# Optimization experiments

Measured on AMD Instinct MI355X. Metric: run time of the kernel, lower is better.

Reference implementation:

```python
import jax, jax.numpy as jnp
import numpy as np

B, N, F_IN, F_OUT, E = 8, 4096, 256, 256, 131072


def setup_inputs() -> dict:
    key = jax.random.key(0)
    kx, ke, kw = jax.random.split(key, 3)
    x = jax.random.normal(kx, (B, N, F_IN), dtype=jnp.float32)
    edge_index = jax.random.randint(ke, (2, E), 0, N, dtype=jnp.int32)
    # Xavier-uniform init for weight, zeros for bias (matches reset_parameters)
    limit = float(np.sqrt(6.0 / (F_IN + F_OUT)))
    weight = jax.random.uniform(kw, (F_IN, F_OUT), dtype=jnp.float32,
                                minval=-limit, maxval=limit)
    bias = jnp.zeros((F_OUT,), dtype=jnp.float32)
    return {"x": x, "edge_index": edge_index, "weight": weight, "bias": bias}


def reference(x, edge_index, weight, bias):
    # x: (B, N, F_in) -> transformed: (B, N, F_out)
    xt = jnp.einsum("bnf,fo->bno", x, weight)
    n_nodes = x.shape[1]
    # Adjacency is identical for every batch element in the original
    # (built from the same edge_index inside the loop) -> build once.
    # .set(1.0) matches torch's `adj[src, dst] = 1.0` (duplicates collapse).
    adj = jnp.zeros((n_nodes, n_nodes), dtype=xt.dtype)
    adj = adj.at[edge_index[0], edge_index[1]].set(1.0)
    degree = adj.sum(axis=1, keepdims=True) + 1e-6  # (N, 1)
    adj_norm = adj / degree
    # Aggregate: out[b] = adj_norm @ xt[b], batched as one einsum
    out = jnp.einsum("ij,bjf->bif", adj_norm, xt)
    return out + bias
```

## Files before the change

### kernel.cpp

```cpp
#include <hip/hip_runtime.h>
#include <hip/hip_bf16.h>


#define GC_B     8
#define GC_N     4096
#define GC_F     256
#define GC_E     131072
#define GC_M     (GC_B * GC_N)
#define MASK_WPR (GC_N / 32)
#define LIST_CAP 128

typedef __attribute__((ext_vector_type(8))) short         short8;
typedef __attribute__((ext_vector_type(2))) float         float2v;
typedef __attribute__((ext_vector_type(4))) float         float4v;
typedef __attribute__((ext_vector_type(4))) unsigned int  uint4v;

static __device__ __forceinline__ unsigned short f2bf_rne(float f) {
    unsigned u = __builtin_bit_cast(unsigned, f);
    u += 0x7fffu + ((u >> 16) & 1u);
    return (unsigned short)(u >> 16);
}

static __device__ __forceinline__ float2v bfpair(unsigned v) {
    return (float2v){__builtin_bit_cast(float, v << 16),
                     __builtin_bit_cast(float, v)};
}

__global__ __launch_bounds__(256) void prep_kernel(
        const float* __restrict__ X, const float* __restrict__ W,
        unsigned short* __restrict__ Xb, unsigned short* __restrict__ Wt,
        unsigned* __restrict__ mask, unsigned* __restrict__ cnt) {
    const int blk = blockIdx.x;
    const int t   = threadIdx.x;
    if (blk < 4096) {
        const size_t i = ((size_t)blk * 256 + t) * 8;
        const float4v v0 = *(const float4v*)(X + i);
        const float4v v1 = *(const float4v*)(X + i + 4);
        union { unsigned short h[8]; short8 s; } u;
        u.h[0] = f2bf_rne(v0[0]); u.h[1] = f2bf_rne(v0[1]);
        u.h[2] = f2bf_rne(v0[2]); u.h[3] = f2bf_rne(v0[3]);
        u.h[4] = f2bf_rne(v1[0]); u.h[5] = f2bf_rne(v1[1]);
        u.h[6] = f2bf_rne(v1[2]); u.h[7] = f2bf_rne(v1[3]);
        *(short8*)(Xb + i) = u.s;
    } else if (blk < 4352) {
        const int n = blk - 4096;
        Wt[n * GC_F + t] = f2bf_rne(W[t * GC_F + n]);
    } else if (blk < 4480) {
        const size_t base = ((size_t)(blk - 4352) * 256 + t) * 4;
        const uint4v z = {0, 0, 0, 0};
        #pragma unroll
        for (int j = 0; j < 4; j++) ((uint4v*)mask)[base + j] = z;
    } else {
        const uint4v z = {0, 0, 0, 0};
        #pragma unroll
        for (int j = 0; j < 4; j++) ((uint4v*)cnt)[(size_t)t * 4 + j] = z;
    }
}

__global__ void build_list_kernel(const int* __restrict__ ei,
                                  unsigned* __restrict__ mask,
                                  unsigned* __restrict__ cnt,
                                  unsigned short* __restrict__ list) {
    const int e = blockIdx.x * blockDim.x + threadIdx.x;
    if (e < GC_E) {
        const int s = ei[e];
        const int d = ei[GC_E + e];
        const unsigned bit = 1u << (d & 31);
        const unsigned old = atomicOr(&mask[s * MASK_WPR + (d >> 5)], bit);
        if (!(old & bit)) {
            const unsigned p = atomicAdd(&cnt[s], 1u);
            if (p < LIST_CAP) list[s * LIST_CAP + p] = (unsigned short)d;
        }
    }
}

__global__ __launch_bounds__(256) void aggregate_kernel(
        const unsigned short* __restrict__ Xb, const unsigned* __restrict__ cnt,
        const unsigned short* __restrict__ list,
        unsigned short* __restrict__ aggb) {
    __shared__ unsigned short lst[4][LIST_CAP];
    __shared__ int degs[4];

    const int w    = threadIdx.x >> 6;
    const int lane = threadIdx.x & 63;
    const int b    = blockIdx.x & 7;
    const int i    = (blockIdx.x >> 3) * 4 + w;
    const int bn   = b * GC_N + i;

    if (lane < 16)
        ((uint4v*)lst[w])[lane] = ((const uint4v*)(list + i * LIST_CAP))[lane];
    if (lane == 0) {
        const unsigned c = cnt[i];
        degs[w] = (int)(c < LIST_CAP ? c : LIST_CAP);
    }
    __syncthreads();

    const int deg = degs[w];
    const int fg  = lane & 31;
    const int ks  = lane >> 5;

    const unsigned short* xbase = Xb + ((size_t)b << 20) + fg * 8;

    float2v a0[4] = {}, a1[4] = {}, a2[4] = {}, a3[4] = {};
    int k = ks;
    for (; k + 6 < deg; k += 8) {
        const unsigned o0 = (unsigned)lst[w][k]     << 8;
        const unsigned o1 = (unsigned)lst[w][k + 2] << 8;
        const unsigned o2 = (unsigned)lst[w][k + 4] << 8;
        const unsigned o3 = (unsigned)lst[w][k + 6] << 8;
        const uint4v v0 = *(const uint4v*)(xbase + o0);
        const uint4v v1 = *(const uint4v*)(xbase + o1);
        const uint4v v2 = *(const uint4v*)(xbase + o2);
        const uint4v v3 = *(const uint4v*)(xbase + o3);
        #pragma unroll
        for (int e = 0; e < 4; e++) {
            a0[e] += bfpair(v0[e]);
            a1[e] += bfpair(v1[e]);
            a2[e] += bfpair(v2[e]);
            a3[e] += bfpair(v3[e]);
        }
    }
    for (; k < deg; k += 2) {
        const uint4v v0 = *(const uint4v*)(xbase + ((unsigned)lst[w][k] << 8));
        #pragma unroll
        for (int e = 0; e < 4; e++) a0[e] += bfpair(v0[e]);
    }

    float acc[8];
    #pragma unroll
    for (int e = 0; e < 4; e++) {
        const float2v s = (a0[e] + a1[e]) + (a2[e] + a3[e]);
        acc[2 * e]     = s.x;
        acc[2 * e + 1] = s.y;
    }
    #pragma unroll
    for (int e = 0; e < 8; e++)
        acc[e] += __shfl_xor(acc[e], 32, 64);

    if (ks == 0) {
        const float inv = 1.0f / ((float)deg + 1e-6f);
        uint4v o;
        #pragma unroll
        for (int e = 0; e < 4; e++) {
            const float s0 = acc[2 * e] * inv;
            const float s1 = acc[2 * e + 1] * inv;
            o[e] = (unsigned)f2bf_rne(s0) | ((unsigned)f2bf_rne(s1) << 16);
        }
        *(uint4v*)(aggb + (size_t)bn * GC_F + fg * 8) = o;
    }
}

#define MROWS 128
__global__ __launch_bounds__(256) void gemm_bias_kernel(
        const unsigned short* __restrict__ Ab,
        const unsigned short* __restrict__ Wt,
        const float* __restrict__ bias, float* __restrict__ out) {
    const int lane = threadIdx.x & 63;
    const int r    = lane & 15;
    const int q    = lane >> 4;
    const int f0   = blockIdx.y * 128 + (threadIdx.x >> 6) * 32;

    short8  wfr[2][8];
    float4v bv[2];
    #pragma unroll
    for (int s = 0; s < 2; s++) {
        const unsigned short* wp = Wt + (size_t)(f0 + 16 * s + r) * GC_F + q * 8;
        #pragma unroll
        for (int kc = 0; kc < 8; kc++) wfr[s][kc] = *(const short8*)(wp + kc * 32);
        bv[s] = *(const float4v*)(bias + f0 + 16 * s + 4 * q);
    }

    const int mbase = blockIdx.x * MROWS;
    #pragma unroll 2
    for (int mt = 0; mt < MROWS / 16; mt++) {
        const int m0 = mbase + mt * 16;
        const unsigned short* ap = Ab + (size_t)(m0 + r) * GC_F + q * 8;
        short8 afr[8];
        #pragma unroll
        for (int kc = 0; kc < 8; kc++) afr[kc] = *(const short8*)(ap + kc * 32);
        #pragma unroll
        for (int s = 0; s < 2; s++) {
            float4v acc = {0, 0, 0, 0};
            #pragma unroll
            for (int kc = 0; kc < 8; kc++)
                acc = __builtin_amdgcn_mfma_f32_16x16x32_bf16(
                    wfr[s][kc], afr[kc], acc, 0, 0, 0);
            *(float4v*)(out + (size_t)(m0 + r) * GC_F + f0 + 16 * s + 4 * q) =
                acc + bv[s];
        }
    }
}

extern "C" void kernel_launch(void* const* d_in, const int* in_sizes, int n_in,
                              void* d_out, int out_size, void* d_ws, size_t ws_size,
                              hipStream_t stream) {
    const float* x      = (const float*)d_in[0];
    const int*   ei     = (const int*)d_in[1];
    const float* weight = (const float*)d_in[2];
    const float* bias   = (const float*)d_in[3];
    float*       out    = (float*)d_out;

    char* p = (char*)d_ws;
    unsigned short* aggb = (unsigned short*)p;             p += (size_t)GC_M * GC_F * 2;
    unsigned short* Xb   = (unsigned short*)p;             p += (size_t)GC_M * GC_F * 2;
    unsigned short* Wt   = (unsigned short*)p;             p += (size_t)GC_F * GC_F * 2;
    unsigned*       mask = (unsigned*)p;                   p += (size_t)GC_N * MASK_WPR * 4;
    unsigned*       cnt  = (unsigned*)p;                   p += (size_t)GC_N * 4;
    unsigned short* list = (unsigned short*)p;

    prep_kernel<<<4481, 256, 0, stream>>>(x, weight, Xb, Wt, mask, cnt);

    build_list_kernel<<<(GC_E + 255) / 256, 256, 0, stream>>>(ei, mask, cnt, list);

    aggregate_kernel<<<GC_M / 4, 256, 0, stream>>>(Xb, cnt, list, aggb);

    dim3 ggrid(GC_M / MROWS, GC_F / 128);
    gemm_bias_kernel<<<ggrid, 256, 0, stream>>>(aggb, Wt, bias, out);
}
```

Measured before the change: 150.1 us.

## Fuse sparse aggregation and bf16 GEMM into one kernel via LDS tile

Merges the aggregate and GEMM kernels. Each block aggregates 32 nodes for one batch and writes the normalized bf16 rows into a swizzled LDS tile, then runs MFMA against W to emit the output with bias. This removes the intermediate aggb round trip through global memory and one kernel launch. In exchange W fragments are reloaded per block, each wave processes 8 nodes serially, and the output stores become nontemporal.

```diff
diff --git a/kernel.cpp b/kernel.cpp
--- a/kernel.cpp
+++ b/kernel.cpp
@@ -9,6 +9,7 @@
 #define GC_M     (GC_B * GC_N)
 #define MASK_WPR (GC_N / 32)
 #define LIST_CAP 128
+#define NPB      32
 
 typedef __attribute__((ext_vector_type(8))) short         short8;
 typedef __attribute__((ext_vector_type(2))) float         float2v;
@@ -74,119 +75,132 @@
     }
 }
 
-__global__ __launch_bounds__(256) void aggregate_kernel(
+__global__ __launch_bounds__(256, 4) void agg_gemm_kernel(
         const unsigned short* __restrict__ Xb, const unsigned* __restrict__ cnt,
         const unsigned short* __restrict__ list,
-        unsigned short* __restrict__ aggb) {
-    __shared__ unsigned short lst[4][LIST_CAP];
-    __shared__ int degs[4];
-
-    const int w    = threadIdx.x >> 6;
-    const int lane = threadIdx.x & 63;
-    const int b    = blockIdx.x & 7;
-    const int i    = (blockIdx.x >> 3) * 4 + w;
-    const int bn   = b * GC_N + i;
-
-    if (lane < 16)
-        ((uint4v*)lst[w])[lane] = ((const uint4v*)(list + i * LIST_CAP))[lane];
-    if (lane == 0) {
-        const unsigned c = cnt[i];
-        degs[w] = (int)(c < LIST_CAP ? c : LIST_CAP);
-    }
-    __syncthreads();
-
-    const int deg = degs[w];
-    const int fg  = lane & 31;
-    const int ks  = lane >> 5;
-
-    const unsigned short* xbase = Xb + ((size_t)b << 20) + fg * 8;
-
-    float2v a0[4] = {}, a1[4] = {}, a2[4] = {}, a3[4] = {};
-    int k = ks;
-    for (; k + 6 < deg; k += 8) {
-        const unsigned o0 = (unsigned)lst[w][k]     << 8;
-        const unsigned o1 = (unsigned)lst[w][k + 2] << 8;
-        const unsigned o2 = (unsigned)lst[w][k + 4] << 8;
-        const unsigned o3 = (unsigned)lst[w][k + 6] << 8;
-        const uint4v v0 = *(const uint4v*)(xbase + o0);
-        const uint4v v1 = *(const uint4v*)(xbase + o1);
-        const uint4v v2 = *(const uint4v*)(xbase + o2);
-        const uint4v v3 = *(const uint4v*)(xbase + o3);
-        #pragma unroll
-        for (int e = 0; e < 4; e++) {
-            a0[e] += bfpair(v0[e]);
-            a1[e] += bfpair(v1[e]);
-            a2[e] += bfpair(v2[e]);
-            a3[e] += bfpair(v3[e]);
-        }
-    }
-    for (; k < deg; k += 2) {
-        const uint4v v0 = *(const uint4v*)(xbase + ((unsigned)lst[w][k] << 8));
-        #pragma unroll
-        for (int e = 0; e < 4; e++) a0[e] += bfpair(v0[e]);
-    }
-
-    float acc[8];
-    #pragma unroll
-    for (int e = 0; e < 4; e++) {
-        const float2v s = (a0[e] + a1[e]) + (a2[e] + a3[e]);
-        acc[2 * e]     = s.x;
-        acc[2 * e + 1] = s.y;
-    }
-    #pragma unroll
-    for (int e = 0; e < 8; e++)
-        acc[e] += __shfl_xor(acc[e], 32, 64);
-
-    if (ks == 0) {
-        const float inv = 1.0f / ((float)deg + 1e-6f);
-        uint4v o;
-        #pragma unroll
-        for (int e = 0; e < 4; e++) {
-            const float s0 = acc[2 * e] * inv;
-            const float s1 = acc[2 * e + 1] * inv;
-            o[e] = (unsigned)f2bf_rne(s0) | ((unsigned)f2bf_rne(s1) << 16);
-        }
-        *(uint4v*)(aggb + (size_t)bn * GC_F + fg * 8) = o;
-    }
-}
-
-#define MROWS 128
-__global__ __launch_bounds__(256) void gemm_bias_kernel(
-        const unsigned short* __restrict__ Ab,
         const unsigned short* __restrict__ Wt,
         const float* __restrict__ bias, float* __restrict__ out) {
-    const int lane = threadIdx.x & 63;
-    const int r    = lane & 15;
-    const int q    = lane >> 4;
-    const int f0   = blockIdx.y * 128 + (threadIdx.x >> 6) * 32;
-
-    short8  wfr[2][8];
-    float4v bv[2];
-    #pragma unroll
-    for (int s = 0; s < 2; s++) {
-        const unsigned short* wp = Wt + (size_t)(f0 + 16 * s + r) * GC_F + q * 8;
-        #pragma unroll
-        for (int kc = 0; kc < 8; kc++) wfr[s][kc] = *(const short8*)(wp + kc * 32);
-        bv[s] = *(const float4v*)(bias + f0 + 16 * s + 4 * q);
-    }
-
-    const int mbase = blockIdx.x * MROWS;
-    #pragma unroll 2
-    for (int mt = 0; mt < MROWS / 16; mt++) {
-        const int m0 = mbase + mt * 16;
-        const unsigned short* ap = Ab + (size_t)(m0 + r) * GC_F + q * 8;
-        short8 afr[8];
-        #pragma unroll
-        for (int kc = 0; kc < 8; kc++) afr[kc] = *(const short8*)(ap + kc * 32);
-        #pragma unroll
-        for (int s = 0; s < 2; s++) {
+    __shared__ __attribute__((aligned(16))) uint4v lstv[NPB * LIST_CAP / 8];
+    __shared__ int degs[NPB];
+    __shared__ __attribute__((aligned(16))) uint4v frag[NPB * GC_F / 8];
+
+    const int tid  = threadIdx.x;
+    const int w    = tid >> 6;
+    const int lane = tid & 63;
+    const int b    = blockIdx.x & 7;
+    const int n0   = (blockIdx.x >> 3) * NPB;
+
+    {
+        const uint4v* src = (const uint4v*)(list + (size_t)n0 * LIST_CAP);
+        lstv[tid]       = src[tid];
+        lstv[tid + 256] = src[tid + 256];
+    }
+    if (tid < NPB) {
+        const unsigned c = cnt[n0 + tid];
+        degs[tid] = (int)(c < LIST_CAP ? c : LIST_CAP);
+    }
+    __syncthreads();
+
+    const unsigned short* lst = (const unsigned short*)lstv;
+    const int fg = lane & 31;
+    const int ks = lane >> 5;
+    const unsigned short* xbase = Xb + ((size_t)b << 20) + fg * 8;
+
+    #pragma unroll 1
+    for (int it = 0; it < 8; ++it) {
+        const int t   = w * 8 + it;
+        const int deg = degs[t];
+        const unsigned short* tl = lst + t * LIST_CAP;
+
+        float2v a0[4] = {}, a1[4] = {}, a2[4] = {}, a3[4] = {};
+        int k = ks;
+        for (; k + 6 < deg; k += 8) {
+            const unsigned o0 = (unsigned)tl[k]     << 8;
+            const unsigned o1 = (unsigned)tl[k + 2] << 8;
+            const unsigned o2 = (unsigned)tl[k + 4] << 8;
+            const unsigned o3 = (unsigned)tl[k + 6] << 8;
+            const uint4v v0 = *(const uint4v*)(xbase + o0);
+            const uint4v v1 = *(const uint4v*)(xbase + o1);
+            const uint4v v2 = *(const uint4v*)(xbase + o2);
+            const uint4v v3 = *(const uint4v*)(xbase + o3);
+            #pragma unroll
+            for (int e = 0; e < 4; e++) {
+                a0[e] += bfpair(v0[e]);
+                a1[e] += bfpair(v1[e]);
+                a2[e] += bfpair(v2[e]);
+                a3[e] += bfpair(v3[e]);
+            }
+        }
+        for (; k < deg; k += 2) {
+            const uint4v v0 = *(const uint4v*)(xbase + ((unsigned)tl[k] << 8));
+            #pragma unroll
+            for (int e = 0; e < 4; e++) a0[e] += bfpair(v0[e]);
+        }
+
+        float accv[8];
+        #pragma unroll
+        for (int e = 0; e < 4; e++) {
+            const float2v s = (a0[e] + a1[e]) + (a2[e] + a3[e]);
+            accv[2 * e]     = s.x;
+            accv[2 * e + 1] = s.y;
+        }
+        #pragma unroll
+        for (int e = 0; e < 8; e++)
+            accv[e] += __shfl_xor(accv[e], 32, 64);
+
+        if (ks == 0) {
+            const float inv = 1.0f / ((float)deg + 1e-6f);
+            uint4v o;
+            #pragma unroll
+            for (int e = 0; e < 4; e++) {
+                const float s0 = accv[2 * e] * inv;
+                const float s1 = accv[2 * e + 1] * inv;
+                o[e] = (unsigned)f2bf_rne(s0) | ((unsigned)f2bf_rne(s1) << 16);
+            }
+            const int mt = t >> 4, r = t & 15;
+            frag[mt * 512 + fg * 16 + (r ^ (fg & 15))] = o;
+        }
+    }
+
+    const int r     = lane & 15;
+    const int q     = lane >> 4;
+    const int fbase = w * 64;
+    short8 wfr[8];
+    {
+        const unsigned short* wp = Wt + (size_t)(fbase + r) * GC_F + q * 8;
+        #pragma unroll
+        for (int kc = 0; kc < 8; kc++) wfr[kc] = *(const short8*)(wp + kc * 32);
+    }
+    __syncthreads();
+
+    const size_t orow0 = ((size_t)b << 12) + n0;
+    const unsigned short* fragb = (const unsigned short*)frag;
+    #pragma unroll 1
+    for (int ft = 0; ft < 4; ++ft) {
+        const int f0 = fbase + ft * 16;
+        const float4v bv = *(const float4v*)(bias + f0 + 4 * q);
+        #pragma unroll
+        for (int mt = 0; mt < 2; mt++) {
+            short8 afr[8];
+            #pragma unroll
+            for (int kc = 0; kc < 8; kc++) {
+                const int ch = 4 * kc + q;
+                afr[kc] = *(const short8*)(fragb + mt * 4096 + ch * 128 +
+                                           (r ^ (ch & 15)) * 8);
+            }
             float4v acc = {0, 0, 0, 0};
             #pragma unroll
             for (int kc = 0; kc < 8; kc++)
                 acc = __builtin_amdgcn_mfma_f32_16x16x32_bf16(
-                    wfr[s][kc], afr[kc], acc, 0, 0, 0);
-            *(float4v*)(out + (size_t)(m0 + r) * GC_F + f0 + 16 * s + 4 * q) =
-                acc + bv[s];
+                    wfr[kc], afr[kc], acc, 0, 0, 0);
+            const float4v res = acc + bv;
+            __builtin_nontemporal_store(res,
+                (float4v*)(out + (orow0 + mt * 16 + r) * GC_F + f0 + 4 * q));
+        }
+        if (ft < 3) {
+            const unsigned short* wp = Wt + (size_t)(f0 + 16 + r) * GC_F + q * 8;
+            #pragma unroll
+            for (int kc = 0; kc < 8; kc++) wfr[kc] = *(const short8*)(wp + kc * 32);
         }
     }
 }
@@ -201,7 +215,6 @@
     float*       out    = (float*)d_out;
 
     char* p = (char*)d_ws;
-    unsigned short* aggb = (unsigned short*)p;             p += (size_t)GC_M * GC_F * 2;
     unsigned short* Xb   = (unsigned short*)p;             p += (size_t)GC_M * GC_F * 2;
     unsigned short* Wt   = (unsigned short*)p;             p += (size_t)GC_F * GC_F * 2;
     unsigned*       mask = (unsigned*)p;                   p += (size_t)GC_N * MASK_WPR * 4;
@@ -212,8 +225,6 @@
 
     build_list_kernel<<<(GC_E + 255) / 256, 256, 0, stream>>>(ei, mask, cnt, list);
 
-    aggregate_kernel<<<GC_M / 4, 256, 0, stream>>>(Xb, cnt, list, aggb);
-
-    dim3 ggrid(GC_M / MROWS, GC_F / 128);
-    gemm_bias_kernel<<<ggrid, 256, 0, stream>>>(aggb, Wt, bias, out);
-}
+    agg_gemm_kernel<<<GC_B * (GC_N / NPB), 256, 0, stream>>>(
+        Xb, cnt, list, Wt, bias, out);
+}
```

Result: no change. 147.4 us (-1.7%).
